# Kernel tuning notes

Measured on AMD Instinct MI355X. Metric: run time of the kernel, lower is better.

The kernel has to match this reference:

```python
import jax, jax.numpy as jnp
import numpy as np

H = 512
INPUT_DIM = 13
OUTPUT_DIM = 1
W_DIM = (INPUT_DIM + OUTPUT_DIM) * H  # 7168
R = 256
N = 2048
LOG_2PI = float(np.log(2.0 * np.pi))


def setup_inputs() -> dict:
    key = jax.random.key(0)
    k1, k2, k3 = jax.random.split(key, 3)
    x = jax.random.normal(k1, (N, INPUT_DIM), dtype=jnp.float32)
    y = jax.random.normal(k2, (N, OUTPUT_DIM), dtype=jnp.float32)
    w = jax.random.normal(k3, (R, W_DIM), dtype=jnp.float32)
    return {"x": x, "y": y, "w": w}


def reference(x, y, w):
    # Batched version of FFReLU.loglik: for each weight sample r,
    #   w1 = w[r, :H*13].reshape(H, 13); w2 = w[r, H*13:].reshape(1, H)
    #   mu = w2 @ relu(w1 @ x.T)            -> [1, N]
    #   logprob[r] = Normal(mu.T, 1).log_prob(y).T
    w1_dim = H * INPUT_DIM
    w1 = w[:, :w1_dim].reshape(R, H, INPUT_DIM)       # [R, H, 13]
    w2 = w[:, w1_dim:].reshape(R, H)                  # [R, H] (output_dim = 1)
    hidden = jax.nn.relu(jnp.einsum('rhi,ni->rnh', w1, x))  # [R, N, H]
    mu = jnp.einsum('rnh,rh->rn', hidden, w2)         # [R, N]
    resid = y[:, 0][None, :] - mu                     # [R, N]
    log_p = -0.5 * resid * resid - 0.5 * LOG_2PI      # Normal(mu, 1) log-prob
    return log_p
```

## Files before the change

kernel.cpp:

```cpp
#include <hip/hip_runtime.h>

#define HH 512
#define IND 13
#define NN 2048
#define RR 256
#define WDIM 7168
#define W1DIM 6656
#define NBLK 256
#define NT 4
#define NTHREADS 256
#define NEG_HALF_LOG_2PI (-0.91893853320467274f)

#define XPK_BYTES   (NN * 32 * 2)
#define W1PK_OFF    XPK_BYTES
#define W1PK_BYTES  (RR * HH * 16 * 2)
#define W2PK_OFF    (W1PK_OFF + W1PK_BYTES)
#define W2PK_BYTES  (RR * HH * 4)
#define WS_NEEDED   (W2PK_OFF + W2PK_BYTES)

typedef __attribute__((ext_vector_type(8))) short short8;
typedef __attribute__((ext_vector_type(4))) float f32x4;
typedef __attribute__((ext_vector_type(2))) float f32x2;

__device__ __forceinline__ short f2bf(float f) {
    unsigned u = __float_as_uint(f);
    u += 0x7fffu + ((u >> 16) & 1u);
    return (short)(u >> 16);
}

#define GLDS16(gsrc, ldst) \
    __builtin_amdgcn_global_load_lds( \
        (const __attribute__((address_space(1))) void*)(gsrc), \
        (__attribute__((address_space(3))) void*)(ldst), 16, 0, 0)


__global__ __launch_bounds__(NTHREADS)
void prep_kernel(const float* __restrict__ x, const float* __restrict__ w,
                 short* __restrict__ xpk, short* __restrict__ w1pk,
                 float* __restrict__ w2pk) {
    const int b = blockIdx.x;
    const int tid = threadIdx.x;
    if (b < 512) {
        const int gid = b * NTHREADS + tid;
        const int r = gid >> 9;
        const int h = gid & 511;
        const float* p = w + (size_t)r * WDIM + (size_t)h * IND;
        short tmp[16];
#pragma unroll
        for (int i = 0; i < 13; ++i) tmp[i] = f2bf(p[i]);
        tmp[13] = 0; tmp[14] = 0; tmp[15] = 0;
        short8* dst = (short8*)(w1pk + (size_t)gid * 16);
        dst[0] = *(short8*)&tmp[0];
        dst[1] = *(short8*)&tmp[8];
        w2pk[gid] = w[(size_t)r * WDIM + W1DIM + h];
    } else {
        const int n = (b - 512) * NTHREADS + tid;
        const float* xp = x + (size_t)n * IND;
        short tmp[32];
#pragma unroll
        for (int i = 0; i < 13; ++i) {
            float v = xp[i];
            unsigned u = __float_as_uint(v);
            tmp[i] = (short)(u >> 16);
            float res = v - __uint_as_float(u & 0xffff0000u);
            tmp[16 + i] = (short)(__float_as_uint(res) >> 16);
        }
        tmp[13] = 0; tmp[14] = 0; tmp[15] = 0;
        tmp[29] = 0; tmp[30] = 0; tmp[31] = 0;
        short8* dst = (short8*)(xpk + (size_t)n * 32);
        dst[0] = *(short8*)&tmp[0];
        dst[1] = *(short8*)&tmp[8];
        dst[2] = *(short8*)&tmp[16];
        dst[3] = *(short8*)&tmp[24];
    }
}

template <bool FROM_WS>
__global__ __launch_bounds__(NTHREADS, 3)
void ffrelu_mfma_kernel(const float* __restrict__ x,
                        const float* __restrict__ y,
                        const float* __restrict__ w,
                        const short* __restrict__ xpk,
                        const short* __restrict__ w1pk,
                        const float* __restrict__ w2pk,
                        float* __restrict__ out) {
    __shared__ short Als[HH * 16];
    __shared__ float w2s[HH];

    const int tid = threadIdx.x;
    const int r = blockIdx.x;
    const int wave = tid >> 6;
    const int lane = tid & 63;
    const int m = lane & 15;
    const int q = lane >> 4;

    if (FROM_WS) {
        const char* w1g = (const char*)(w1pk + (size_t)r * (HH * 16))
                          + wave * 4096 + (size_t)lane * 16;
        char* alsb = (char*)Als + wave * 4096;
#pragma unroll
        for (int i = 0; i < 4; ++i) GLDS16(w1g + i * 1024, alsb + i * 1024);
        if (wave < 2) {
            const char* w2g = (const char*)(w2pk + (size_t)r * HH)
                              + wave * 1024 + (size_t)lane * 16;
            GLDS16(w2g, (char*)w2s + wave * 1024);
        }
    } else {
        const float* wr = w + (size_t)r * WDIM;
#pragma unroll
        for (int rr = 0; rr < 2; ++rr) {
            const int h = tid * 2 + rr;
            const float* p = wr + (size_t)h * IND;
            short tmp[16];
#pragma unroll
            for (int i = 0; i < 13; ++i) tmp[i] = f2bf(p[i]);
            tmp[13] = 0; tmp[14] = 0; tmp[15] = 0;
            *(short8*)&Als[h * 16]     = *(short8*)&tmp[0];
            *(short8*)&Als[h * 16 + 8] = *(short8*)&tmp[8];
        }
        w2s[tid]       = wr[W1DIM + tid];
        w2s[tid + 256] = wr[W1DIM + tid + 256];
    }

    const bool lo  = (q >= 2);
    const bool hi8 = (q & 1);
    const f32x2 zero2 = {0.0f, 0.0f};
    const f32x4 czero = {0.0f, 0.0f, 0.0f, 0.0f};

    const int nb = blockIdx.y * NBLK + wave * 64;
    short8 bfrag[NT];
    if (FROM_WS) {
        const short* base = xpk + (size_t)(nb + m) * 32 + (lo ? 16 : 0) + (hi8 ? 8 : 0);
#pragma unroll
        for (int nt = 0; nt < NT; ++nt) {
            bfrag[nt] = *(const short8*)(base + nt * 16 * 32);
        }
    } else {
#pragma unroll
        for (int nt = 0; nt < NT; ++nt) {
            const float* xp = x + (size_t)(nb + nt * 16 + m) * IND;
            short hs[13], ls[13];
#pragma unroll
            for (int i = 0; i < 13; ++i) {
                float v = xp[i];
                unsigned u = __float_as_uint(v);
                hs[i] = (short)(u >> 16);
                float res = v - __uint_as_float(u & 0xffff0000u);
                ls[i] = (short)(__float_as_uint(res) >> 16);
            }
            short s[13];
#pragma unroll
            for (int i = 0; i < 13; ++i) s[i] = lo ? ls[i] : hs[i];
            short8 b;
            b[0] = hi8 ? s[8]     : s[0];
            b[1] = hi8 ? s[9]     : s[1];
            b[2] = hi8 ? s[10]    : s[2];
            b[3] = hi8 ? s[11]    : s[3];
            b[4] = hi8 ? s[12]    : s[4];
            b[5] = hi8 ? (short)0 : s[5];
            b[6] = hi8 ? (short)0 : s[6];
            b[7] = hi8 ? (short)0 : s[7];
            bfrag[nt] = b;
        }
    }

    const float yv = y[nb + lane];

    __syncthreads();

    f32x2 muv[NT][2];
#pragma unroll
    for (int i = 0; i < NT; ++i) {
        muv[i][0] = zero2;
        muv[i][1] = zero2;
    }

#pragma unroll 2
    for (int t = 0; t < 32; ++t) {
        const short8 a = *(const short8*)&Als[(t * 16 + m) * 16 + (q & 1) * 8];
        const f32x4 wv = *(const f32x4*)&w2s[t * 16 + q * 4];
        const f32x2 wv01 = {wv[0], wv[1]};
        const f32x2 wv23 = {wv[2], wv[3]};
#pragma unroll
        for (int nt = 0; nt < NT; ++nt) {
            f32x4 c = __builtin_amdgcn_mfma_f32_16x16x32_bf16(a, bfrag[nt], czero, 0, 0, 0);
            f32x2 c01 = {c[0], c[1]};
            f32x2 c23 = {c[2], c[3]};
            c01 = __builtin_elementwise_max(c01, zero2);
            c23 = __builtin_elementwise_max(c23, zero2);
            muv[nt][0] += c01 * wv01;
            muv[nt][1] += c23 * wv23;
        }
    }

    float mu[NT];
#pragma unroll
    for (int nt = 0; nt < NT; ++nt) {
        f32x2 p = muv[nt][0] + muv[nt][1];
        float v = p[0] + p[1];
        v += __shfl_xor(v, 16, 64);
        v += __shfl_xor(v, 32, 64);
        mu[nt] = v;
    }

    float mu0;
    if (q == 0)      mu0 = mu[0];
    else if (q == 1) mu0 = mu[1];
    else if (q == 2) mu0 = mu[2];
    else             mu0 = mu[3];

    const int n0 = nb + lane;
    float resid0 = yv - mu0;
    out[(size_t)r * NN + n0] = fmaf(-0.5f * resid0, resid0, NEG_HALF_LOG_2PI);
}

extern "C" void kernel_launch(void* const* d_in, const int* in_sizes, int n_in,
                              void* d_out, int out_size, void* d_ws, size_t ws_size,
                              hipStream_t stream) {
    const float* x = (const float*)d_in[0];
    const float* y = (const float*)d_in[1];
    const float* w = (const float*)d_in[2];
    float* out = (float*)d_out;
    char* ws = (char*)d_ws;
    short* xpk  = (short*)ws;
    short* w1pk = (short*)(ws + W1PK_OFF);
    float* w2pk = (float*)(ws + W2PK_OFF);

    dim3 grid(RR, NN / NBLK);
    dim3 block(NTHREADS);

    if (ws_size >= (size_t)WS_NEEDED) {
        prep_kernel<<<520, NTHREADS, 0, stream>>>(x, w, xpk, w1pk, w2pk);
        ffrelu_mfma_kernel<true><<<grid, block, 0, stream>>>(x, y, w, xpk, w1pk, w2pk, out);
    } else {
        ffrelu_mfma_kernel<false><<<grid, block, 0, stream>>>(x, y, w, xpk, w1pk, w2pk, out);
    }
}
```

Before: 91.65 us.

## Switch hidden-layer GEMM to 32x32x16 MFMA with separate hi/lo bf16 passes

Replaces the 16x16x32 bf16 MFMA, which packed the hi and lo bf16 parts of x into one K=32 operand, with 32x32x16 MFMAs. Each tile now runs two accumulating MFMAs, one for the hi part and one for the lo part. Each wave covers its 64 samples as two 32-column tiles over 16 hidden-tile steps. This changes the fragment layout, the w2 broadcast pattern and the final cross-lane reduction, which shrinks to a single shuffle exchange. The aim is fewer MFMA issues and LDS A-reads per unit of work, at the cost of a larger 16-float accumulator per MFMA and more register pressure.

```diff
diff --git a/kernel.cpp b/kernel.cpp
--- a/kernel.cpp
+++ b/kernel.cpp
@@ -7,7 +7,6 @@
 #define WDIM 7168
 #define W1DIM 6656
 #define NBLK 256
-#define NT 4
 #define NTHREADS 256
 #define NEG_HALF_LOG_2PI (-0.91893853320467274f)
 
@@ -20,6 +19,7 @@
 
 typedef __attribute__((ext_vector_type(8))) short short8;
 typedef __attribute__((ext_vector_type(4))) float f32x4;
+typedef __attribute__((ext_vector_type(16))) float f32x16;
 typedef __attribute__((ext_vector_type(2))) float f32x2;
 
 __device__ __forceinline__ short f2bf(float f) {
@@ -91,8 +91,8 @@
     const int r = blockIdx.x;
     const int wave = tid >> 6;
     const int lane = tid & 63;
-    const int m = lane & 15;
-    const int q = lane >> 4;
+    const int col = lane & 31;
+    const int khalf = lane >> 5;
 
     if (FROM_WS) {
         const char* w1g = (const char*)(w1pk + (size_t)r * (HH * 16))
@@ -122,45 +122,37 @@
         w2s[tid + 256] = wr[W1DIM + tid + 256];
     }
 
-    const bool lo  = (q >= 2);
-    const bool hi8 = (q & 1);
     const f32x2 zero2 = {0.0f, 0.0f};
-    const f32x4 czero = {0.0f, 0.0f, 0.0f, 0.0f};
+    f32x16 czero;
+#pragma unroll
+    for (int i = 0; i < 16; ++i) czero[i] = 0.0f;
 
     const int nb = blockIdx.y * NBLK + wave * 64;
-    short8 bfrag[NT];
+    short8 bhi[2], blo[2];
     if (FROM_WS) {
-        const short* base = xpk + (size_t)(nb + m) * 32 + (lo ? 16 : 0) + (hi8 ? 8 : 0);
-#pragma unroll
-        for (int nt = 0; nt < NT; ++nt) {
-            bfrag[nt] = *(const short8*)(base + nt * 16 * 32);
-        }
-    } else {
-#pragma unroll
-        for (int nt = 0; nt < NT; ++nt) {
-            const float* xp = x + (size_t)(nb + nt * 16 + m) * IND;
-            short hs[13], ls[13];
-#pragma unroll
-            for (int i = 0; i < 13; ++i) {
-                float v = xp[i];
+#pragma unroll
+        for (int nt = 0; nt < 2; ++nt) {
+            const short* base = xpk + (size_t)(nb + nt * 32 + col) * 32 + khalf * 8;
+            bhi[nt] = *(const short8*)(base);
+            blo[nt] = *(const short8*)(base + 16);
+        }
+    } else {
+#pragma unroll
+        for (int nt = 0; nt < 2; ++nt) {
+            const float* xp = x + (size_t)(nb + nt * 32 + col) * IND;
+            short8 bh, bl;
+#pragma unroll
+            for (int i = 0; i < 8; ++i) {
+                const int k = khalf * 8 + i;
+                float v = 0.0f;
+                if (k < 13) v = xp[k];
                 unsigned u = __float_as_uint(v);
-                hs[i] = (short)(u >> 16);
+                bh[i] = (short)(u >> 16);
                 float res = v - __uint_as_float(u & 0xffff0000u);
-                ls[i] = (short)(__float_as_uint(res) >> 16);
+                bl[i] = (short)(__float_as_uint(res) >> 16);
             }
-            short s[13];
-#pragma unroll
-            for (int i = 0; i < 13; ++i) s[i] = lo ? ls[i] : hs[i];
-            short8 b;
-            b[0] = hi8 ? s[8]     : s[0];
-            b[1] = hi8 ? s[9]     : s[1];
-            b[2] = hi8 ? s[10]    : s[2];
-            b[3] = hi8 ? s[11]    : s[3];
-            b[4] = hi8 ? s[12]    : s[4];
-            b[5] = hi8 ? (short)0 : s[5];
-            b[6] = hi8 ? (short)0 : s[6];
-            b[7] = hi8 ? (short)0 : s[7];
-            bfrag[nt] = b;
+            bhi[nt] = bh;
+            blo[nt] = bl;
         }
     }
 
@@ -168,46 +160,47 @@
 
     __syncthreads();
 
-    f32x2 muv[NT][2];
-#pragma unroll
-    for (int i = 0; i < NT; ++i) {
-        muv[i][0] = zero2;
-        muv[i][1] = zero2;
-    }
+    f32x2 muv[2][2];
+#pragma unroll
+    for (int i = 0; i < 2; ++i) { muv[i][0] = zero2; muv[i][1] = zero2; }
 
 #pragma unroll 2
-    for (int t = 0; t < 32; ++t) {
-        const short8 a = *(const short8*)&Als[(t * 16 + m) * 16 + (q & 1) * 8];
-        const f32x4 wv = *(const f32x4*)&w2s[t * 16 + q * 4];
-        const f32x2 wv01 = {wv[0], wv[1]};
-        const f32x2 wv23 = {wv[2], wv[3]};
-#pragma unroll
-        for (int nt = 0; nt < NT; ++nt) {
-            f32x4 c = __builtin_amdgcn_mfma_f32_16x16x32_bf16(a, bfrag[nt], czero, 0, 0, 0);
-            f32x2 c01 = {c[0], c[1]};
-            f32x2 c23 = {c[2], c[3]};
-            c01 = __builtin_elementwise_max(c01, zero2);
-            c23 = __builtin_elementwise_max(c23, zero2);
-            muv[nt][0] += c01 * wv01;
-            muv[nt][1] += c23 * wv23;
-        }
-    }
-
-    float mu[NT];
-#pragma unroll
-    for (int nt = 0; nt < NT; ++nt) {
+    for (int t = 0; t < 16; ++t) {
+        const short8 a = *(const short8*)&Als[(t * 32 + col) * 16 + khalf * 8];
+        f32x16 c0 = __builtin_amdgcn_mfma_f32_32x32x16_bf16(a, bhi[0], czero, 0, 0, 0);
+        c0        = __builtin_amdgcn_mfma_f32_32x32x16_bf16(a, blo[0], c0,    0, 0, 0);
+        f32x16 c1 = __builtin_amdgcn_mfma_f32_32x32x16_bf16(a, bhi[1], czero, 0, 0, 0);
+        c1        = __builtin_amdgcn_mfma_f32_32x32x16_bf16(a, blo[1], c1,    0, 0, 0);
+        const float* w2t = &w2s[t * 32 + khalf * 4];
+#pragma unroll
+        for (int g = 0; g < 4; ++g) {
+            const f32x4 wv = *(const f32x4*)&w2t[g * 8];
+            const f32x2 wv01 = {wv[0], wv[1]};
+            const f32x2 wv23 = {wv[2], wv[3]};
+            f32x2 p01 = {c0[4 * g],     c0[4 * g + 1]};
+            f32x2 p23 = {c0[4 * g + 2], c0[4 * g + 3]};
+            p01 = __builtin_elementwise_max(p01, zero2);
+            p23 = __builtin_elementwise_max(p23, zero2);
+            muv[0][0] += p01 * wv01;
+            muv[0][1] += p23 * wv23;
+            f32x2 q01 = {c1[4 * g],     c1[4 * g + 1]};
+            f32x2 q23 = {c1[4 * g + 2], c1[4 * g + 3]};
+            q01 = __builtin_elementwise_max(q01, zero2);
+            q23 = __builtin_elementwise_max(q23, zero2);
+            muv[1][0] += q01 * wv01;
+            muv[1][1] += q23 * wv23;
+        }
+    }
+
+    float mup[2];
+#pragma unroll
+    for (int nt = 0; nt < 2; ++nt) {
         f32x2 p = muv[nt][0] + muv[nt][1];
-        float v = p[0] + p[1];
-        v += __shfl_xor(v, 16, 64);
-        v += __shfl_xor(v, 32, 64);
-        mu[nt] = v;
-    }
-
-    float mu0;
-    if (q == 0)      mu0 = mu[0];
-    else if (q == 1) mu0 = mu[1];
-    else if (q == 2) mu0 = mu[2];
-    else             mu0 = mu[3];
+        mup[nt] = p[0] + p[1];
+    }
+    const float send = khalf ? mup[0] : mup[1];
+    const float recv = __shfl_xor(send, 32, 64);
+    const float mu0 = (khalf ? mup[1] : mup[0]) + recv;
 
     const int n0 = nb + lane;
     float resid0 = yv - mu0;
```

Result: no change. 92.49 us (+0.9%).
